# Kernel optimization log

Hardware: AMD Instinct MI355X
Metric: run time of the kernel (lower is better)

Reference implementation:

```python
import jax, jax.numpy as jnp
import numpy as np

K = 3            # spline kernel_size per pseudo-coord dim (dim=2 -> K*K=9 weights)
FILTERS = [64, 64, 64]
N_OUT = 10


def _spline_basis(u):
    # u: [B,N,N,2], open degree-1 B-spline basis on pseudo-coords in [0,1]
    v = u * (K - 1)
    i0 = jnp.clip(jnp.floor(v), 0.0, K - 2)
    f = v - i0                                  # fractional part in [0,1]
    i0 = i0.astype(jnp.int32)
    b = (1.0 - f)[..., None] * jax.nn.one_hot(i0, K, dtype=u.dtype) \
        + f[..., None] * jax.nn.one_hot(i0 + 1, K, dtype=u.dtype)   # [B,N,N,2,K]
    basis = b[..., 0, :, None] * b[..., 1, None, :]                  # [B,N,N,K,K]
    return basis.reshape(u.shape[0], u.shape[1], u.shape[2], K * K)  # [B,N,N,9]


def _spline_conv(h, basis_masked, deg, w, root, bias):
    # h: [B,N,Cin]; basis_masked: [B,N,N,9]; w: [9,Cin,Cout]
    hw = jnp.einsum('bmc,kcf->bmkf', h, w)                 # per-kernel transformed feats
    agg = jnp.einsum('bnmk,bmkf->bnf', basis_masked, hw) / deg   # mean neighbor aggregation
    return agg + h @ root + bias


def setup_inputs() -> dict:
    key = jax.random.key(0)
    B, N, C = 32, 512, 128   # C = in_features + 18
    ks = jax.random.split(key, 16)
    x = jax.random.normal(ks[0], (B, N, C), jnp.float32)
    coord = jax.random.uniform(ks[1], (B, N, 2), jnp.float32)
    adj = (jax.random.uniform(ks[2], (B, N, N), jnp.float32) < 0.06).astype(jnp.float32)
    adj = adj * (1.0 - jnp.eye(N, dtype=jnp.float32))  # no self-loops; root weight handles self
    inp = {"x": x, "coord": coord, "adj": adj}
    cin = C
    for l, f in enumerate(FILTERS):
        inp[f"w{l}"] = jax.random.normal(ks[3 + 3 * l], (K * K, cin, f), jnp.float32) / np.float32(np.sqrt(cin * K * K))
        inp[f"root{l}"] = jax.random.normal(ks[4 + 3 * l], (cin, f), jnp.float32) / np.float32(np.sqrt(cin))
        inp[f"b{l}"] = jnp.zeros((f,), jnp.float32)
        cin = f
    inp["fc_w"] = jax.random.normal(ks[13], (FILTERS[-1], N_OUT), jnp.float32) / np.float32(np.sqrt(FILTERS[-1]))
    inp["fc_b"] = jnp.zeros((N_OUT,), jnp.float32)
    return inp


def reference(x, coord, adj, w0, root0, b0, w1, root1, b1, w2, root2, b2, fc_w, fc_b):
    # get_monet_coord: relative 2D offsets of connected nodes, mapped to [0,1]
    u = (coord[:, None, :, :] - coord[:, :, None, :] + 1.0) * 0.5     # [B,N,N,2]
    basis = _spline_basis(u) * adj[..., None]                          # mask to edges
    deg = jnp.clip(jnp.sum(adj, axis=-1, keepdims=True), 1.0, None)   # [B,N,1]
    h = x
    for w, r, b in ((w0, root0, b0), (w1, root1, b1), (w2, root2, b2)):
        h = jax.nn.relu(_spline_conv(h, basis, deg, w, r, b))
    g = jnp.max(h, axis=1)          # global max-pool over nodes -> [B, 64]
    return g @ fc_w + fc_b          # dropout is an inference no-op -> [B, 10]
```

## Files before the change

kernel.cpp:

```cpp
#include <hip/hip_runtime.h>


#define B_   32
#define N_   512
#define F_   64
#define CAP  128

typedef float f32x4 __attribute__((ext_vector_type(4)));
typedef _Float16 f16x8 __attribute__((ext_vector_type(8)));
typedef _Float16 f16x2 __attribute__((ext_vector_type(2)));

__global__ __launch_bounds__(512, 8) void preprocess_kernel(
    const float* __restrict__ adj, const float* __restrict__ coord,
    int* __restrict__ edge_m, float4* __restrict__ edge_w,
    int4* __restrict__ cnt4,
    float* __restrict__ deginv, unsigned int* __restrict__ gmax,
    const float* __restrict__ x, _Float16* __restrict__ hx,
    const float* __restrict__ w0, const float* __restrict__ root0,
    const float* __restrict__ w1, const float* __restrict__ root1,
    const float* __restrict__ w2, const float* __restrict__ root2,
    _Float16* __restrict__ wt0, _Float16* __restrict__ wt1,
    _Float16* __restrict__ wt2) {
  int tid = threadIdx.x, wave = tid >> 6, lane = tid & 63;
  if (tid == 0) gmax[blockIdx.x] = 0u;

  {
    int idx = blockIdx.x * 512 + tid;
    const int CX = B_ * N_ * 32;
    const int S0 = 64 * 1280, S1 = 64 * 640;
    if (idx < CX) {
      float4 v = ((const float4*)x)[idx];
      f16x2 p0, p1;
      p0[0] = (_Float16)v.x; p0[1] = (_Float16)v.y;
      p1[0] = (_Float16)v.z; p1[1] = (_Float16)v.w;
      uint2 u;
      u.x = __builtin_bit_cast(unsigned, p0);
      u.y = __builtin_bit_cast(unsigned, p1);
      ((uint2*)hx)[idx] = u;
    } else if (idx < CX + S0 + 2 * S1) {
      int r = idx - CX;
      const float *w, *root; _Float16* wt; int KP, CIN;
      if (r < S0)           { w = w0; root = root0; wt = wt0; KP = 1280; CIN = 128; }
      else if (r < S0 + S1) { w = w1; root = root1; wt = wt1; KP = 640;  CIN = 64;  r -= S0; }
      else                  { w = w2; root = root2; wt = wt2; KP = 640;  CIN = 64;  r -= S0 + S1; }
      int f = r / KP, k = r - f * KP;
      int ks = k / CIN, c = k - ks * CIN;
      float v = (ks < 9) ? w[((size_t)ks * CIN + c) * F_ + f]
                         : root[(size_t)c * F_ + f];
      wt[(size_t)f * KP + k] = (_Float16)v;
    }
  }

  int row = blockIdx.x * 8 + wave;
  int b = row >> 9;
  float cxn = coord[(size_t)row * 2 + 0];
  float cyn = coord[(size_t)row * 2 + 1];

  int   pq[8];
  float pfx[8], pfy[8];
  int q0 = 0, q1 = 0, q2 = 0, q3 = 0;
  #pragma unroll
  for (int c = 0; c < 8; ++c) {
    int m = c * 64 + lane;
    float a = adj[(size_t)row * N_ + m];
    bool flag = (a != 0.0f);
    float cxm = coord[(size_t)(b * N_ + m) * 2 + 0];
    float cym = coord[(size_t)(b * N_ + m) * 2 + 1];
    float vx = cxm - cxn + 1.0f;
    float vy = cym - cyn + 1.0f;
    float i0x = fminf(fmaxf(floorf(vx), 0.0f), 1.0f);
    float i0y = fminf(fmaxf(floorf(vy), 0.0f), 1.0f);
    pfx[c] = vx - i0x;
    pfy[c] = vy - i0y;
    int quad = (int)i0x + 2 * (int)i0y;
    pq[c] = flag ? quad : -1;
    q0 += __popcll(__ballot(flag && quad == 0));
    q1 += __popcll(__ballot(flag && quad == 1));
    q2 += __popcll(__ballot(flag && quad == 2));
    q3 += __popcll(__ballot(flag && quad == 3));
  }
  int qt0 = q0, qt1 = q0 + q1, qt2 = qt1 + q2, qt3 = qt2 + q3;

  int ro0 = 0, ro1 = qt0, ro2 = qt1, ro3 = qt2;
  #pragma unroll
  for (int c = 0; c < 8; ++c) {
    unsigned long long b0 = __ballot(pq[c] == 0);
    unsigned long long b1 = __ballot(pq[c] == 1);
    unsigned long long b2 = __ballot(pq[c] == 2);
    unsigned long long b3 = __ballot(pq[c] == 3);
    int q = pq[c];
    if (q >= 0) {
      unsigned long long myb = (q == 0) ? b0 : (q == 1) ? b1 : (q == 2) ? b2 : b3;
      int base = (q == 0) ? ro0 : (q == 1) ? ro1 : (q == 2) ? ro2 : ro3;
      int off = base + __popcll(myb & ((1ULL << lane) - 1ULL));
      if (off < CAP) {
        float fx = pfx[c], fy = pfy[c];
        float gx = 1.0f - fx, gy = 1.0f - fy;
        edge_m[(size_t)row * CAP + off] = c * 64 + lane;
        edge_w[(size_t)row * CAP + off] =
            make_float4(gx * gy, gx * fy, fx * gy, fx * fy);
      }
    }
    ro0 += __popcll(b0); ro1 += __popcll(b1);
    ro2 += __popcll(b2); ro3 += __popcll(b3);
  }
  if (lane == 0) {
    int C0 = min(qt0, CAP), C1 = min(qt1, CAP);
    int C2 = min(qt2, CAP), C3c = min(qt3, CAP);
    cnt4[row] = make_int4(C0, C1 - C0, C2 - C1, C3c - C2);
    deginv[row] = 1.0f / (float)(qt3 > 0 ? qt3 : 1);
  }
}

template<int CH>
__global__ __launch_bounds__(256, 8) void gather_kernel(
    const _Float16* __restrict__ hsrc,
    const int* __restrict__ edge_m, const float4* __restrict__ edge_w,
    const int4* __restrict__ cnt4,
    const float* __restrict__ deginv,
    _Float16* __restrict__ sp) {
  const int CIN = 64 * CH, KP = 10 * CIN;
  __shared__ float4 eshw[4][CAP];
  __shared__ int eshm[4][CAP];
  int wave = threadIdx.x >> 6, lane = threadIdx.x & 63;
  int xcd = blockIdx.x & 7;
  int j = blockIdx.x >> 3;
  int b = xcd * 4 + (j >> 7);
  int n = ((j & 127) << 2) + wave;
  int row = (b << 9) + n;
  int4 c4 = cnt4[row];
  int e1 = c4.x, e2 = e1 + c4.y, e3 = e2 + c4.z, e4 = e3 + c4.w;
  size_t ebase = (size_t)row * CAP;
  for (int i = lane; i < e4; i += 64) {
    eshw[wave][i] = edge_w[ebase + i];
    eshm[wave][i] = edge_m[ebase + i];
  }
  float di = deginv[row];
  const _Float16* hb = hsrc + (size_t)b * N_ * CIN + lane * CH;

  float acc[3][3][CH];
  #pragma unroll
  for (int kx = 0; kx < 3; ++kx)
    #pragma unroll
    for (int ky = 0; ky < 3; ++ky)
      #pragma unroll
      for (int c = 0; c < CH; ++c) acc[kx][ky][c] = 0.0f;

#define EDGE_BODY(E, KX, KY) {                                        \
    int m = eshm[wave][E];                                            \
    float4 wv = eshw[wave][E];                                        \
    float hv[CH];                                                     \
    if (CH == 1) {                                                    \
      hv[0] = (float)hb[(size_t)m * 64];                              \
    } else {                                                          \
      unsigned u = *(const unsigned*)&hb[(size_t)m * 128];            \
      f16x2 hp = __builtin_bit_cast(f16x2, u);                        \
      hv[0] = (float)hp[0]; hv[CH - 1] = (float)hp[1];                \
    }                                                                 \
    _Pragma("unroll")                                                 \
    for (int c = 0; c < CH; ++c) {                                    \
      acc[KX][KY][c]         += wv.x * hv[c];                         \
      acc[KX][KY + 1][c]     += wv.y * hv[c];                         \
      acc[KX + 1][KY][c]     += wv.z * hv[c];                         \
      acc[KX + 1][KY + 1][c] += wv.w * hv[c];                         \
    } }

  #pragma unroll 4
  for (int e = 0; e < e1; ++e) EDGE_BODY(e, 0, 0)
  #pragma unroll 4
  for (int e = e1; e < e2; ++e) EDGE_BODY(e, 1, 0)
  #pragma unroll 4
  for (int e = e2; e < e3; ++e) EDGE_BODY(e, 0, 1)
  #pragma unroll 4
  for (int e = e3; e < e4; ++e) EDGE_BODY(e, 1, 1)
#undef EDGE_BODY

  _Float16* sr = sp + (size_t)row * KP + lane * CH;
  #pragma unroll
  for (int kx = 0; kx < 3; ++kx)
    #pragma unroll
    for (int ky = 0; ky < 3; ++ky) {
      int k = kx * 3 + ky;
      if (CH == 1) {
        sr[(size_t)k * CIN] = (_Float16)(acc[kx][ky][0] * di);
      } else {
        f16x2 p;
        p[0] = (_Float16)(acc[kx][ky][0] * di);
        p[1] = (_Float16)(acc[kx][ky][CH - 1] * di);
        *(f16x2*)&sr[(size_t)k * CIN] = p;
      }
    }
  if (CH == 1) {
    sr[(size_t)9 * CIN] = hb[(size_t)n * 64];
  } else {
    *(unsigned*)&sr[(size_t)9 * CIN] = *(const unsigned*)&hb[(size_t)n * 128];
  }
}

#define GBK  64
#define GLDK 72
__global__ __launch_bounds__(256) void gemm_s_kernel(
    const _Float16* __restrict__ A, const _Float16* __restrict__ Wt,
    const float* __restrict__ bias, _Float16* __restrict__ hout,
    unsigned int* __restrict__ gmax, int KP) {
  __shared__ __attribute__((aligned(16))) _Float16 As[2][64 * GLDK];
  __shared__ __attribute__((aligned(16))) _Float16 Ws[2][64 * GLDK];
  int bm = blockIdx.x << 6;
  int tid = threadIdx.x, wave = tid >> 6, lane = tid & 63;
  int lr = lane & 15, quad = lane >> 4;
  int srow = tid >> 3, sck = (tid & 7) * 8;
  const size_t aoff = (size_t)(bm + srow) * KP + sck;
  const size_t woff = (size_t)srow * KP + sck;

  f32x4 acc[4] = {};
  {
    *(float4*)&As[0][srow * GLDK + sck]        = *(const float4*)&A[aoff];
    *(float4*)&As[0][(srow + 32) * GLDK + sck] = *(const float4*)&A[aoff + (size_t)32 * KP];
    *(float4*)&Ws[0][srow * GLDK + sck]        = *(const float4*)&Wt[woff];
    *(float4*)&Ws[0][(srow + 32) * GLDK + sck] = *(const float4*)&Wt[woff + (size_t)32 * KP];
  }
  int S = KP / GBK, cur = 0;
  float4 pa0, pa1, pw0, pw1;
  for (int s = 0; s < S; ++s) {
    if (s + 1 < S) {
      int k0 = (s + 1) * GBK;
      pa0 = *(const float4*)&A[aoff + k0];
      pa1 = *(const float4*)&A[aoff + (size_t)32 * KP + k0];
      pw0 = *(const float4*)&Wt[woff + k0];
      pw1 = *(const float4*)&Wt[woff + (size_t)32 * KP + k0];
    }
    __syncthreads();
    #pragma unroll
    for (int kk = 0; kk < GBK; kk += 32) {
      f16x8 af = *(const f16x8*)&As[cur][(16 * wave + lr) * GLDK + kk + quad * 8];
      #pragma unroll
      for (int j = 0; j < 4; ++j) {
        f16x8 bf = *(const f16x8*)&Ws[cur][(16 * j + lr) * GLDK + kk + quad * 8];
        acc[j] = __builtin_amdgcn_mfma_f32_16x16x32_f16(af, bf, acc[j], 0, 0, 0);
      }
    }
    if (s + 1 < S) {
      int nb = cur ^ 1;
      *(float4*)&As[nb][srow * GLDK + sck]        = pa0;
      *(float4*)&As[nb][(srow + 32) * GLDK + sck] = pa1;
      *(float4*)&Ws[nb][srow * GLDK + sck]        = pw0;
      *(float4*)&Ws[nb][(srow + 32) * GLDK + sck] = pw1;
    }
    cur ^= 1;
  }
  int b = bm >> 9;
  #pragma unroll
  for (int j = 0; j < 4; ++j) {
    int f = 16 * j + lr;
    float bs = bias[f];
    float vmax = 0.0f;
    #pragma unroll
    for (int r = 0; r < 4; ++r) {
      int m = bm + (wave << 4) + (quad << 2) + r;
      float v = fmaxf(acc[j][r] + bs, 0.0f);
      if (hout) hout[(size_t)m * F_ + f] = (_Float16)v;
      vmax = fmaxf(vmax, v);
    }
    if (gmax) atomicMax(&gmax[(b << 6) + f], __float_as_uint(vmax));
  }
}

__global__ __launch_bounds__(64) void fc_kernel(
    const float* __restrict__ g, const float* __restrict__ fcw,
    const float* __restrict__ fcb, float* __restrict__ out) {
  int b = blockIdx.x;
  int f = threadIdx.x;
  __shared__ float gs[64];
  gs[f] = g[b * F_ + f];
  __syncthreads();
  if (f < 10) {
    float s = fcb[f];
    #pragma unroll
    for (int c = 0; c < 64; ++c) s += gs[c] * fcw[c * 10 + f];
    out[b * 10 + f] = s;
  }
}

extern "C" void kernel_launch(void* const* d_in, const int* in_sizes, int n_in,
                              void* d_out, int out_size, void* d_ws, size_t ws_size,
                              hipStream_t stream) {
  const float* x     = (const float*)d_in[0];
  const float* coord = (const float*)d_in[1];
  const float* adj   = (const float*)d_in[2];
  const float* w0    = (const float*)d_in[3];
  const float* root0 = (const float*)d_in[4];
  const float* b0    = (const float*)d_in[5];
  const float* w1    = (const float*)d_in[6];
  const float* root1 = (const float*)d_in[7];
  const float* b1    = (const float*)d_in[8];
  const float* w2    = (const float*)d_in[9];
  const float* root2 = (const float*)d_in[10];
  const float* b2    = (const float*)d_in[11];
  const float* fcw   = (const float*)d_in[12];
  const float* fcb   = (const float*)d_in[13];
  float* out = (float*)d_out;

  char* ws = (char*)d_ws;
  size_t off = 0;
  auto alloc = [&](size_t bytes) {
    void* p = ws + off;
    off = (off + bytes + 255) & ~(size_t)255;
    return p;
  };
  const int R = B_ * N_;
  int*    edge_m  = (int*)   alloc((size_t)R * CAP * 4);
  float4* edge_w  = (float4*)alloc((size_t)R * CAP * 16);
  int4*   cnt4    = (int4*)  alloc((size_t)R * 16);
  float*  deginv  = (float*) alloc((size_t)R * 4);
  _Float16* hx    = (_Float16*)alloc((size_t)R * 128 * 2);
  _Float16* wt0   = (_Float16*)alloc((size_t)64 * 1280 * 2);
  _Float16* wt1   = (_Float16*)alloc((size_t)64 * 640 * 2);
  _Float16* wt2   = (_Float16*)alloc((size_t)64 * 640 * 2);
  _Float16* sp    = (_Float16*)alloc((size_t)R * 1280 * 2);
  _Float16* hA    = (_Float16*)alloc((size_t)R * 64 * 2);
  _Float16* hB    = (_Float16*)alloc((size_t)R * 64 * 2);
  unsigned int* gmax = (unsigned int*)alloc((size_t)B_ * F_ * 4);

  preprocess_kernel<<<R / 8, 512, 0, stream>>>(
      adj, coord, edge_m, edge_w, cnt4, deginv, gmax,
      x, hx, w0, root0, w1, root1, w2, root2, wt0, wt1, wt2);

  gather_kernel<2><<<R / 4, 256, 0, stream>>>(hx, edge_m, edge_w, cnt4, deginv, sp);
  gemm_s_kernel<<<R / 64, 256, 0, stream>>>(sp, wt0, b0, hA, nullptr, 1280);

  gather_kernel<1><<<R / 4, 256, 0, stream>>>(hA, edge_m, edge_w, cnt4, deginv, sp);
  gemm_s_kernel<<<R / 64, 256, 0, stream>>>(sp, wt1, b1, hB, nullptr, 640);

  gather_kernel<1><<<R / 4, 256, 0, stream>>>(hB, edge_m, edge_w, cnt4, deginv, sp);
  gemm_s_kernel<<<R / 64, 256, 0, stream>>>(sp, wt2, b2, nullptr, gmax, 640);

  fc_kernel<<<B_, 64, 0, stream>>>((const float*)gmax, fcw, fcb, out);
}
```

Before: 213.8 us.

## Fuse gather with per-block MFMA GEMM, removing the sp intermediate buffer

Merges the gather kernel and the dense GEMM into one kernel. Each block gathers the aggregated spline features for its 4 rows into shared memory, then runs a 16x16x32 MFMA over the full K dimension against weights read straight from global memory. This drops the large sp round trip through global memory and three kernel launches. In exchange the MFMA tile is mostly wasted, since only 4 of 16 rows are real, and each block re-reads the whole weight matrix from L2.

```diff
diff --git a/kernel.cpp b/kernel.cpp
--- a/kernel.cpp
+++ b/kernel.cpp
@@ -113,21 +113,26 @@
 }
 
 template<int CH>
-__global__ __launch_bounds__(256, 8) void gather_kernel(
+__global__ __launch_bounds__(256, 8) void fused_kernel(
     const _Float16* __restrict__ hsrc,
     const int* __restrict__ edge_m, const float4* __restrict__ edge_w,
     const int4* __restrict__ cnt4,
     const float* __restrict__ deginv,
-    _Float16* __restrict__ sp) {
-  const int CIN = 64 * CH, KP = 10 * CIN;
+    const _Float16* __restrict__ Wt,
+    const float* __restrict__ bias,
+    _Float16* __restrict__ hout,
+    unsigned int* __restrict__ gmax) {
+  const int CIN = 64 * CH, KP = 10 * CIN, SLD = KP + 8;
   __shared__ float4 eshw[4][CAP];
   __shared__ int eshm[4][CAP];
+  __shared__ __attribute__((aligned(16))) _Float16 st[4][SLD];
   int wave = threadIdx.x >> 6, lane = threadIdx.x & 63;
   int xcd = blockIdx.x & 7;
   int j = blockIdx.x >> 3;
   int b = xcd * 4 + (j >> 7);
   int n = ((j & 127) << 2) + wave;
   int row = (b << 9) + n;
+  int rowbase = row - wave;
   int4 c4 = cnt4[row];
   int e1 = c4.x, e2 = e1 + c4.y, e3 = e2 + c4.z, e4 = e3 + c4.w;
   size_t ebase = (size_t)row * CAP;
@@ -175,93 +180,48 @@
   for (int e = e3; e < e4; ++e) EDGE_BODY(e, 1, 1)
 #undef EDGE_BODY
 
-  _Float16* sr = sp + (size_t)row * KP + lane * CH;
   #pragma unroll
   for (int kx = 0; kx < 3; ++kx)
     #pragma unroll
     for (int ky = 0; ky < 3; ++ky) {
       int k = kx * 3 + ky;
       if (CH == 1) {
-        sr[(size_t)k * CIN] = (_Float16)(acc[kx][ky][0] * di);
+        st[wave][k * CIN + lane] = (_Float16)(acc[kx][ky][0] * di);
       } else {
         f16x2 p;
         p[0] = (_Float16)(acc[kx][ky][0] * di);
         p[1] = (_Float16)(acc[kx][ky][CH - 1] * di);
-        *(f16x2*)&sr[(size_t)k * CIN] = p;
+        *(f16x2*)&st[wave][k * CIN + lane * CH] = p;
       }
     }
   if (CH == 1) {
-    sr[(size_t)9 * CIN] = hb[(size_t)n * 64];
+    st[wave][9 * CIN + lane] = hb[(size_t)n * 64];
   } else {
-    *(unsigned*)&sr[(size_t)9 * CIN] = *(const unsigned*)&hb[(size_t)n * 128];
-  }
-}
-
-#define GBK  64
-#define GLDK 72
-__global__ __launch_bounds__(256) void gemm_s_kernel(
-    const _Float16* __restrict__ A, const _Float16* __restrict__ Wt,
-    const float* __restrict__ bias, _Float16* __restrict__ hout,
-    unsigned int* __restrict__ gmax, int KP) {
-  __shared__ __attribute__((aligned(16))) _Float16 As[2][64 * GLDK];
-  __shared__ __attribute__((aligned(16))) _Float16 Ws[2][64 * GLDK];
-  int bm = blockIdx.x << 6;
-  int tid = threadIdx.x, wave = tid >> 6, lane = tid & 63;
+    *(unsigned*)&st[wave][9 * CIN + lane * 2] = *(const unsigned*)&hb[(size_t)n * 128];
+  }
+  __syncthreads();
+
   int lr = lane & 15, quad = lane >> 4;
-  int srow = tid >> 3, sck = (tid & 7) * 8;
-  const size_t aoff = (size_t)(bm + srow) * KP + sck;
-  const size_t woff = (size_t)srow * KP + sck;
-
-  f32x4 acc[4] = {};
-  {
-    *(float4*)&As[0][srow * GLDK + sck]        = *(const float4*)&A[aoff];
-    *(float4*)&As[0][(srow + 32) * GLDK + sck] = *(const float4*)&A[aoff + (size_t)32 * KP];
-    *(float4*)&Ws[0][srow * GLDK + sck]        = *(const float4*)&Wt[woff];
-    *(float4*)&Ws[0][(srow + 32) * GLDK + sck] = *(const float4*)&Wt[woff + (size_t)32 * KP];
-  }
-  int S = KP / GBK, cur = 0;
-  float4 pa0, pa1, pw0, pw1;
-  for (int s = 0; s < S; ++s) {
-    if (s + 1 < S) {
-      int k0 = (s + 1) * GBK;
-      pa0 = *(const float4*)&A[aoff + k0];
-      pa1 = *(const float4*)&A[aoff + (size_t)32 * KP + k0];
-      pw0 = *(const float4*)&Wt[woff + k0];
-      pw1 = *(const float4*)&Wt[woff + (size_t)32 * KP + k0];
-    }
-    __syncthreads();
-    #pragma unroll
-    for (int kk = 0; kk < GBK; kk += 32) {
-      f16x8 af = *(const f16x8*)&As[cur][(16 * wave + lr) * GLDK + kk + quad * 8];
-      #pragma unroll
-      for (int j = 0; j < 4; ++j) {
-        f16x8 bf = *(const f16x8*)&Ws[cur][(16 * j + lr) * GLDK + kk + quad * 8];
-        acc[j] = __builtin_amdgcn_mfma_f32_16x16x32_f16(af, bf, acc[j], 0, 0, 0);
-      }
-    }
-    if (s + 1 < S) {
-      int nb = cur ^ 1;
-      *(float4*)&As[nb][srow * GLDK + sck]        = pa0;
-      *(float4*)&As[nb][(srow + 32) * GLDK + sck] = pa1;
-      *(float4*)&Ws[nb][srow * GLDK + sck]        = pw0;
-      *(float4*)&Ws[nb][(srow + 32) * GLDK + sck] = pw1;
-    }
-    cur ^= 1;
-  }
-  int b = bm >> 9;
-  #pragma unroll
-  for (int j = 0; j < 4; ++j) {
-    int f = 16 * j + lr;
-    float bs = bias[f];
+  int fcol = (wave << 4) + lr;
+  const _Float16* wrow = Wt + (size_t)fcol * KP + quad * 8;
+  const _Float16* arow = &st[lr & 3][quad * 8];
+  f32x4 oacc = {0.f, 0.f, 0.f, 0.f};
+  #pragma unroll 4
+  for (int ks = 0; ks < KP; ks += 32) {
+    f16x8 af = *(const f16x8*)(arow + ks);
+    f16x8 bf = *(const f16x8*)(wrow + ks);
+    oacc = __builtin_amdgcn_mfma_f32_16x16x32_f16(af, bf, oacc, 0, 0, 0);
+  }
+  if (quad == 0) {
+    float bs = bias[fcol];
     float vmax = 0.0f;
     #pragma unroll
     for (int r = 0; r < 4; ++r) {
-      int m = bm + (wave << 4) + (quad << 2) + r;
-      float v = fmaxf(acc[j][r] + bs, 0.0f);
-      if (hout) hout[(size_t)m * F_ + f] = (_Float16)v;
+      float v = fmaxf(oacc[r] + bs, 0.0f);
+      if (hout) hout[(size_t)(rowbase + r) * F_ + fcol] = (_Float16)v;
       vmax = fmaxf(vmax, v);
     }
-    if (gmax) atomicMax(&gmax[(b << 6) + f], __float_as_uint(vmax));
+    if (gmax) atomicMax(&gmax[(b << 6) + fcol], __float_as_uint(vmax));
   }
 }
 
@@ -316,7 +276,6 @@
   _Float16* wt0   = (_Float16*)alloc((size_t)64 * 1280 * 2);
   _Float16* wt1   = (_Float16*)alloc((size_t)64 * 640 * 2);
   _Float16* wt2   = (_Float16*)alloc((size_t)64 * 640 * 2);
-  _Float16* sp    = (_Float16*)alloc((size_t)R * 1280 * 2);
   _Float16* hA    = (_Float16*)alloc((size_t)R * 64 * 2);
   _Float16* hB    = (_Float16*)alloc((size_t)R * 64 * 2);
   unsigned int* gmax = (unsigned int*)alloc((size_t)B_ * F_ * 4);
@@ -325,14 +284,12 @@
       adj, coord, edge_m, edge_w, cnt4, deginv, gmax,
       x, hx, w0, root0, w1, root1, w2, root2, wt0, wt1, wt2);
 
-  gather_kernel<2><<<R / 4, 256, 0, stream>>>(hx, edge_m, edge_w, cnt4, deginv, sp);
-  gemm_s_kernel<<<R / 64, 256, 0, stream>>>(sp, wt0, b0, hA, nullptr, 1280);
-
-  gather_kernel<1><<<R / 4, 256, 0, stream>>>(hA, edge_m, edge_w, cnt4, deginv, sp);
-  gemm_s_kernel<<<R / 64, 256, 0, stream>>>(sp, wt1, b1, hB, nullptr, 640);
-
-  gather_kernel<1><<<R / 4, 256, 0, stream>>>(hB, edge_m, edge_w, cnt4, deginv, sp);
-  gemm_s_kernel<<<R / 64, 256, 0, stream>>>(sp, wt2, b2, nullptr, gmax, 640);
+  fused_kernel<2><<<R / 4, 256, 0, stream>>>(hx, edge_m, edge_w, cnt4, deginv,
+                                             wt0, b0, hA, nullptr);
+  fused_kernel<1><<<R / 4, 256, 0, stream>>>(hA, edge_m, edge_w, cnt4, deginv,
+                                             wt1, b1, hB, nullptr);
+  fused_kernel<1><<<R / 4, 256, 0, stream>>>(hB, edge_m, edge_w, cnt4, deginv,
+                                             wt2, b2, nullptr, gmax);
 
   fc_kernel<<<B_, 64, 0, stream>>>((const float*)gmax, fcw, fcb, out);
 }
```

Result: slower. 291.5 us (+36.4%).

## Pad per-quadrant edge lists to multiples of four and software-pipeline gather loads

Applied to the files above, without the earlier changes.

The preprocess kernel now pads each quadrant's edge segment up to a multiple of four, filling the padding with zero-weight dummy edges that point to node 0, and stores the padded counts. The gather kernel then handles edges in groups of four with double-buffered register prefetch: it loads the next group's neighbor features while it accumulates the current group. This is meant to hide global-load latency and remove per-edge loop overhead. In exchange it does extra dummy work on padding and rebudgets the CAP truncation across quadrants, which can change which edges are kept in rows near capacity.

```diff
diff --git a/kernel.cpp b/kernel.cpp
--- a/kernel.cpp
+++ b/kernel.cpp
@@ -79,9 +79,17 @@
     q2 += __popcll(__ballot(flag && quad == 2));
     q3 += __popcll(__ballot(flag && quad == 3));
   }
-  int qt0 = q0, qt1 = q0 + q1, qt2 = qt1 + q2, qt3 = qt2 + q3;
-
-  int ro0 = 0, ro1 = qt0, ro2 = qt1, ro3 = qt2;
+
+  int rem = CAP;
+  int c0 = min(q0, rem); int c0p = min((c0 + 3) & ~3, rem); rem -= c0p;
+  int c1 = min(q1, rem); int c1p = min((c1 + 3) & ~3, rem); rem -= c1p;
+  int c2 = min(q2, rem); int c2p = min((c2 + 3) & ~3, rem); rem -= c2p;
+  int c3 = min(q3, rem); int c3p = min((c3 + 3) & ~3, rem);
+  c0 = min(c0, c0p); c1 = min(c1, c1p); c2 = min(c2, c2p); c3 = min(c3, c3p);
+  int B1 = c0p, B2 = c0p + c1p, B3 = B2 + c2p;
+  int L0 = c0, L1 = B1 + c1, L2 = B2 + c2, L3 = B3 + c3;
+
+  int ro0 = 0, ro1 = B1, ro2 = B2, ro3 = B3;
   #pragma unroll
   for (int c = 0; c < 8; ++c) {
     unsigned long long b0 = __ballot(pq[c] == 0);
@@ -92,8 +100,9 @@
     if (q >= 0) {
       unsigned long long myb = (q == 0) ? b0 : (q == 1) ? b1 : (q == 2) ? b2 : b3;
       int base = (q == 0) ? ro0 : (q == 1) ? ro1 : (q == 2) ? ro2 : ro3;
+      int lim  = (q == 0) ? L0  : (q == 1) ? L1  : (q == 2) ? L2  : L3;
       int off = base + __popcll(myb & ((1ULL << lane) - 1ULL));
-      if (off < CAP) {
+      if (off < lim) {
         float fx = pfx[c], fy = pfy[c];
         float gx = 1.0f - fx, gy = 1.0f - fy;
         edge_m[(size_t)row * CAP + off] = c * 64 + lane;
@@ -104,11 +113,20 @@
     ro0 += __popcll(b0); ro1 += __popcll(b1);
     ro2 += __popcll(b2); ro3 += __popcll(b3);
   }
+  if (lane < 16) {
+    int q = lane >> 2, i = lane & 3;
+    int cq  = (q == 0) ? c0  : (q == 1) ? c1  : (q == 2) ? c2  : c3;
+    int cqp = (q == 0) ? c0p : (q == 1) ? c1p : (q == 2) ? c2p : c3p;
+    int Bq  = (q == 0) ? 0   : (q == 1) ? B1  : (q == 2) ? B2  : B3;
+    if (cq + i < cqp) {
+      edge_m[(size_t)row * CAP + Bq + cq + i] = 0;
+      edge_w[(size_t)row * CAP + Bq + cq + i] = make_float4(0.f, 0.f, 0.f, 0.f);
+    }
+  }
   if (lane == 0) {
-    int C0 = min(qt0, CAP), C1 = min(qt1, CAP);
-    int C2 = min(qt2, CAP), C3c = min(qt3, CAP);
-    cnt4[row] = make_int4(C0, C1 - C0, C2 - C1, C3c - C2);
-    deginv[row] = 1.0f / (float)(qt3 > 0 ? qt3 : 1);
+    cnt4[row] = make_int4(c0p, c1p, c2p, c3p);
+    int total = q0 + q1 + q2 + q3;
+    deginv[row] = 1.0f / (float)(total > 0 ? total : 1);
   }
 }
 
@@ -146,15 +164,30 @@
       #pragma unroll
       for (int c = 0; c < CH; ++c) acc[kx][ky][c] = 0.0f;
 
-#define EDGE_BODY(E, KX, KY) {                                        \
-    int m = eshm[wave][E];                                            \
+#define LOADH(P, G) {                                                 \
+    int m0 = eshm[wave][(G) + 0];                                     \
+    int m1 = eshm[wave][(G) + 1];                                     \
+    int m2 = eshm[wave][(G) + 2];                                     \
+    int m3 = eshm[wave][(G) + 3];                                     \
+    if (CH == 1) {                                                    \
+      P##0 = *(const unsigned short*)&hb[(size_t)m0 * 64];            \
+      P##1 = *(const unsigned short*)&hb[(size_t)m1 * 64];            \
+      P##2 = *(const unsigned short*)&hb[(size_t)m2 * 64];            \
+      P##3 = *(const unsigned short*)&hb[(size_t)m3 * 64];            \
+    } else {                                                          \
+      P##0 = *(const unsigned*)&hb[(size_t)m0 * 128];                 \
+      P##1 = *(const unsigned*)&hb[(size_t)m1 * 128];                 \
+      P##2 = *(const unsigned*)&hb[(size_t)m2 * 128];                 \
+      P##3 = *(const unsigned*)&hb[(size_t)m3 * 128];                 \
+    } }
+
+#define CONS1(U, E, KX, KY) {                                         \
     float4 wv = eshw[wave][E];                                        \
     float hv[CH];                                                     \
     if (CH == 1) {                                                    \
-      hv[0] = (float)hb[(size_t)m * 64];                              \
+      hv[0] = (float)__builtin_bit_cast(_Float16, (unsigned short)(U));\
     } else {                                                          \
-      unsigned u = *(const unsigned*)&hb[(size_t)m * 128];            \
-      f16x2 hp = __builtin_bit_cast(f16x2, u);                        \
+      f16x2 hp = __builtin_bit_cast(f16x2, (unsigned)(U));            \
       hv[0] = (float)hp[0]; hv[CH - 1] = (float)hp[1];                \
     }                                                                 \
     _Pragma("unroll")                                                 \
@@ -165,15 +198,31 @@
       acc[KX + 1][KY + 1][c] += wv.w * hv[c];                         \
     } }
 
-  #pragma unroll 4
-  for (int e = 0; e < e1; ++e) EDGE_BODY(e, 0, 0)
-  #pragma unroll 4
-  for (int e = e1; e < e2; ++e) EDGE_BODY(e, 1, 0)
-  #pragma unroll 4
-  for (int e = e2; e < e3; ++e) EDGE_BODY(e, 0, 1)
-  #pragma unroll 4
-  for (int e = e3; e < e4; ++e) EDGE_BODY(e, 1, 1)
-#undef EDGE_BODY
+#define CONSG(P, G, KX, KY) {                                         \
+    CONS1(P##0, (G) + 0, KX, KY); CONS1(P##1, (G) + 1, KX, KY);       \
+    CONS1(P##2, (G) + 2, KX, KY); CONS1(P##3, (G) + 3, KX, KY); }
+
+#define QUAD_LOOP(QS, QE, KX, KY) {                                   \
+    int g = (QS);                                                     \
+    if (g < (QE)) {                                                   \
+      unsigned A0, A1, A2, A3, B0, B1, B2, B3;                        \
+      LOADH(A, g);                                                    \
+      for (; g + 4 < (QE); g += 4) {                                  \
+        LOADH(B, g + 4);                                              \
+        CONSG(A, g, KX, KY);                                          \
+        A0 = B0; A1 = B1; A2 = B2; A3 = B3;                           \
+      }                                                               \
+      CONSG(A, g, KX, KY);                                            \
+    } }
+
+  QUAD_LOOP(0, e1, 0, 0)
+  QUAD_LOOP(e1, e2, 1, 0)
+  QUAD_LOOP(e2, e3, 0, 1)
+  QUAD_LOOP(e3, e4, 1, 1)
+#undef QUAD_LOOP
+#undef CONSG
+#undef CONS1
+#undef LOADH
 
   _Float16* sr = sp + (size_t)row * KP + lane * CH;
   #pragma unroll
```

After: 230.5 us. +7.9%, slower.
